# Kernel tuning notes

Hardware: AMD Instinct MI355X
Metric: run time of the kernel (lower is better)

## Reference

```python
import jax, jax.numpy as jnp
import numpy as np
from jax import lax

CHAOS_R = 3.5699456
N_STEPS = 10


def setup_inputs() -> dict:
    key = jax.random.key(0)
    k1, k2, k3 = jax.random.split(key, 3)
    B, T, D = 256, 8192, 5
    x = jax.random.normal(k1, (B, T, D), dtype=jnp.float32)
    temple = jax.random.normal(k2, (4, 5), dtype=jnp.float32)
    breath_vector = jax.random.normal(k3, (5,), dtype=jnp.float32)
    return {"x": x, "temple": temple, "breath_vector": breath_vector}


def reference(x, temple, breath_vector):
    # x: (B, T, D) with D == 5
    B, T, D = x.shape

    # mirror_sequence: chaos logistic map on mean of x[0,0]
    seed = jnp.mod(jnp.mean(x[0, 0]), 1.0)
    chaos = CHAOS_R * seed * (1.0 - seed)
    mirrored = jnp.where(chaos > 0.7, 9.0 - x,
                         jnp.where(chaos > 0.4, jnp.flip(x, axis=1), x))
    mode_code = jnp.where(chaos > 0.7, 0, jnp.where(chaos > 0.4, 1, 2))  # 0=invert,1=retrograde,2=none

    extended_x = jnp.concatenate([x, mirrored], axis=1)  # (B, 2T, D)

    # per-token breath: first T tokens use breath[:4], mirrored half uses breath[1:5]
    breath_main = breath_vector[:4]
    breath_mirror = breath_vector[1:5]
    breath = jnp.concatenate([
        jnp.broadcast_to(breath_main, (T, 4)),
        jnp.broadcast_to(breath_mirror, (T, 4)),
    ], axis=0)  # (2T, 4)

    def step(vec, _):
        # vec: (B, 2T, 5)
        transformed = jnp.einsum('rd,btd->btr', temple, vec)  # (B, 2T, 4)
        resonance = jnp.sum(transformed * breath[None, :, :], axis=-1)  # (B, 2T)
        vec = jnp.roll(vec, shift=1, axis=-1).at[..., 0].set(jnp.mod(resonance, 10.0))
        return vec, resonance

    vec0 = extended_x[..., :5]
    _, history = lax.scan(step, vec0, None, length=N_STEPS)  # (10, B, 2T)

    # torch.std default is unbiased (ddof=1)
    score = 1.0 / (1.0 + jnp.std(history, axis=0, ddof=1))  # (B, 2T)
    gate_weights = score[..., None]  # (B, 2T, 1)
    return gate_weights, extended_x, mode_code
```

## Files before the change

kernel.cpp:

```cpp
#include <hip/hip_runtime.h>

constexpr int B_DIM = 256, T_DIM = 8192;
constexpr long long GATE_N = (long long)B_DIM * 2 * T_DIM;
constexpr long long EXT_N  = GATE_N * 5;

__global__ void temple_setup(const float* __restrict__ x, const float* __restrict__ temple,
                             const float* __restrict__ breath,
                             float* __restrict__ out, double* __restrict__ w) {
    if (threadIdx.x != 0) return;
    double s = 0.0;
    for (int d = 0; d < 5; ++d) s += (double)x[d];
    s = s / 5.0;
    double seed  = s - floor(s);
    double chaos = 3.5699456 * seed * (1.0 - seed);
    int mode = (chaos > 0.7) ? 0 : ((chaos > 0.4) ? 1 : 2);
    for (int d = 0; d < 5; ++d) {
        double a = 0.0, c = 0.0;
        for (int r = 0; r < 4; ++r) {
            double tv = (double)temple[r * 5 + d];
            a += (double)breath[r]     * tv;
            c += (double)breath[r + 1] * tv;
        }
        w[d] = a; w[5 + d] = c;
    }
    w[10] = (double)mode;
    out[GATE_N + EXT_N] = (float)mode;
}

__global__ __launch_bounds__(256) void temple_main(const float* __restrict__ x,
                                                   const double* __restrict__ w,
                                                   float* __restrict__ out) {
    const int k  = threadIdx.x;
    const int b  = blockIdx.x >> 5;
    const int t0 = (blockIdx.x & 31) << 8;
    const int mode = (int)w[10];
    const long long rowBase = (long long)b * (2 * T_DIM);
    float* gate = out;
    float* ext  = out + GATE_N;

    const float4* __restrict__ src4 = (const float4*)(x + ((long long)b * T_DIM + t0) * 5);
    const bool extra = (k < 64);
    float4 c0 = src4[k];
    float4 c1;
    if (extra) c1 = src4[256 + k];

    float4* dmain = (float4*)(ext + (rowBase + t0) * 5);
    dmain[k] = c0;
    if (extra) dmain[256 + k] = c1;
    if (mode == 0) {
        float4* dmir = (float4*)(ext + (rowBase + T_DIM + t0) * 5);
        dmir[k] = make_float4(9.f - c0.x, 9.f - c0.y, 9.f - c0.z, 9.f - c0.w);
        if (extra) dmir[256 + k] = make_float4(9.f - c1.x, 9.f - c1.y, 9.f - c1.z, 9.f - c1.w);
    } else if (mode == 2) {
        float4* dmir = (float4*)(ext + (rowBase + T_DIM + t0) * 5);
        dmir[k] = c0;
        if (extra) dmir[256 + k] = c1;
    }

    const int t = t0 + k;
    const float* __restrict__ xi = x + ((long long)b * T_DIM + t) * 5;
    const float x0 = xi[0], x1 = xi[1], x2 = xi[2], x3 = xi[3], x4 = xi[4];

    if (mode == 1) {
        float* dm = ext + (rowBase + 2 * T_DIM - 1 - t) * 5;
        dm[0] = x0; dm[1] = x1; dm[2] = x2; dm[3] = x3; dm[4] = x4;
    }

    const double wa0 = w[0], wa1 = w[1], wa2 = w[2], wa3 = w[3], wa4 = w[4];
    const double wb0 = w[5], wb1 = w[6], wb2 = w[7], wb3 = w[8], wb4 = w[9];
    double a0 = x0, a1 = x1, a2 = x2, a3 = x3, a4 = x4;
    double b0, b1, b2, b3, b4;
    if (mode == 0) { b0 = 9.0 - a0; b1 = 9.0 - a1; b2 = 9.0 - a2; b3 = 9.0 - a3; b4 = 9.0 - a4; }
    else           { b0 = a0; b1 = a1; b2 = a2; b3 = a3; b4 = a4; }

    float ha[10], hb[10];
#pragma unroll
    for (int s = 0; s < 10; ++s) {
        double ra = a0 * wa0;
        ra = fma(a1, wa1, ra); ra = fma(a2, wa2, ra); ra = fma(a3, wa3, ra); ra = fma(a4, wa4, ra);
        double rb = b0 * wb0;
        rb = fma(b1, wb1, rb); rb = fma(b2, wb2, rb); rb = fma(b3, wb3, rb); rb = fma(b4, wb4, rb);
        ha[s] = (float)ra; hb[s] = (float)rb;
        double qa = floor(ra * 0.1), ma = fma(qa, -10.0, ra);
        ma = (ma < 0.0) ? ma + 10.0 : ma;  ma = (ma >= 10.0) ? ma - 10.0 : ma;
        double qb = floor(rb * 0.1), mb = fma(qb, -10.0, rb);
        mb = (mb < 0.0) ? mb + 10.0 : mb;  mb = (mb >= 10.0) ? mb - 10.0 : mb;
        a4 = a3; a3 = a2; a2 = a1; a1 = a0; a0 = ma;
        b4 = b3; b3 = b2; b2 = b1; b1 = b0; b0 = mb;
    }
    float meanA = 0.f, meanB = 0.f;
#pragma unroll
    for (int s = 0; s < 10; ++s) { meanA += ha[s]; meanB += hb[s]; }
    meanA *= 0.1f; meanB *= 0.1f;
    float ssdA = 0.f, ssdB = 0.f;
#pragma unroll
    for (int s = 0; s < 10; ++s) {
        float da = ha[s] - meanA; ssdA = fmaf(da, da, ssdA);
        float db = hb[s] - meanB; ssdB = fmaf(db, db, ssdB);
    }
    const float gm = 1.0f / (1.0f + sqrtf(ssdA * (1.0f / 9.0f)));
    const float gx = 1.0f / (1.0f + sqrtf(ssdB * (1.0f / 9.0f)));

    gate[rowBase + t] = gm;
    if (mode == 1) gate[rowBase + 2 * T_DIM - 1 - t] = gx;
    else           gate[rowBase + T_DIM + t] = gx;
}

extern "C" void kernel_launch(void* const* d_in, const int* in_sizes, int n_in,
                              void* d_out, int out_size, void* d_ws, size_t ws_size,
                              hipStream_t stream) {
    const float* x      = (const float*)d_in[0];
    const float* temple = (const float*)d_in[1];
    const float* breath = (const float*)d_in[2];
    float* out = (float*)d_out;
    double* w  = (double*)d_ws;

    temple_setup<<<1, 64, 0, stream>>>(x, temple, breath, out, w);
    const int blocks = (B_DIM * T_DIM) / 256;
    temple_main<<<blocks, 256, 0, stream>>>(x, w, out);
}
```

Before: 143.1 us.

## Split copy and gate computation into separate kernels, use one-pass variance

The fused kernel is split in two. One kernel copies the input into the extended output with float4 loads and stores, including a vectorized gather for the retrograde mode. A second kernel computes the gate values. The gate kernel drops the 10-element history arrays and computes variance in one pass from running sum and sum of squares, clamping negatives to zero. This trades an extra launch and a second read of x for simpler kernels with fewer registers, at some risk to numerical accuracy from the one-pass variance formula.

```diff
diff --git a/kernel.cpp b/kernel.cpp
--- a/kernel.cpp
+++ b/kernel.cpp
@@ -27,44 +27,45 @@
     out[GATE_N + EXT_N] = (float)mode;
 }
 
-__global__ __launch_bounds__(256) void temple_main(const float* __restrict__ x,
+__global__ __launch_bounds__(256) void temple_copy(const float* __restrict__ x,
                                                    const double* __restrict__ w,
                                                    float* __restrict__ out) {
-    const int k  = threadIdx.x;
-    const int b  = blockIdx.x >> 5;
-    const int t0 = (blockIdx.x & 31) << 8;
+    const int b = blockIdx.x / 40;
+    const int j = (blockIdx.x - b * 40) * 256 + threadIdx.x;
+    const int mode = (int)w[10];
+
+    const float4 v = ((const float4*)x)[(long long)b * 10240 + j];
+    float4* dst = (float4*)(out + GATE_N) + (long long)b * 20480;
+    dst[j] = v;
+
+    if (mode == 0) {
+        dst[10240 + j] = make_float4(9.f - v.x, 9.f - v.y, 9.f - v.z, 9.f - v.w);
+    } else if (mode == 2) {
+        dst[10240 + j] = v;
+    } else {
+        const float* __restrict__ xr = x + (long long)b * 40960;
+        float vv[4];
+#pragma unroll
+        for (int c = 0; c < 4; ++c) {
+            const int fl = j * 4 + c;
+            const int d  = fl % 5;
+            vv[c] = xr[40955 - fl + 2 * d];
+        }
+        dst[10240 + j] = make_float4(vv[0], vv[1], vv[2], vv[3]);
+    }
+}
+
+__global__ __launch_bounds__(256) void temple_gate(const float* __restrict__ x,
+                                                   const double* __restrict__ w,
+                                                   float* __restrict__ out) {
+    const long long tid = (long long)blockIdx.x * 256 + threadIdx.x;
+    const int b = (int)(tid >> 13);
+    const int t = (int)(tid & (T_DIM - 1));
     const int mode = (int)w[10];
     const long long rowBase = (long long)b * (2 * T_DIM);
-    float* gate = out;
-    float* ext  = out + GATE_N;
 
-    const float4* __restrict__ src4 = (const float4*)(x + ((long long)b * T_DIM + t0) * 5);
-    const bool extra = (k < 64);
-    float4 c0 = src4[k];
-    float4 c1;
-    if (extra) c1 = src4[256 + k];
-
-    float4* dmain = (float4*)(ext + (rowBase + t0) * 5);
-    dmain[k] = c0;
-    if (extra) dmain[256 + k] = c1;
-    if (mode == 0) {
-        float4* dmir = (float4*)(ext + (rowBase + T_DIM + t0) * 5);
-        dmir[k] = make_float4(9.f - c0.x, 9.f - c0.y, 9.f - c0.z, 9.f - c0.w);
-        if (extra) dmir[256 + k] = make_float4(9.f - c1.x, 9.f - c1.y, 9.f - c1.z, 9.f - c1.w);
-    } else if (mode == 2) {
-        float4* dmir = (float4*)(ext + (rowBase + T_DIM + t0) * 5);
-        dmir[k] = c0;
-        if (extra) dmir[256 + k] = c1;
-    }
-
-    const int t = t0 + k;
     const float* __restrict__ xi = x + ((long long)b * T_DIM + t) * 5;
     const float x0 = xi[0], x1 = xi[1], x2 = xi[2], x3 = xi[3], x4 = xi[4];
-
-    if (mode == 1) {
-        float* dm = ext + (rowBase + 2 * T_DIM - 1 - t) * 5;
-        dm[0] = x0; dm[1] = x1; dm[2] = x2; dm[3] = x3; dm[4] = x4;
-    }
 
     const double wa0 = w[0], wa1 = w[1], wa2 = w[2], wa3 = w[3], wa4 = w[4];
     const double wb0 = w[5], wb1 = w[6], wb2 = w[7], wb3 = w[8], wb4 = w[9];
@@ -73,14 +74,16 @@
     if (mode == 0) { b0 = 9.0 - a0; b1 = 9.0 - a1; b2 = 9.0 - a2; b3 = 9.0 - a3; b4 = 9.0 - a4; }
     else           { b0 = a0; b1 = a1; b2 = a2; b3 = a3; b4 = a4; }
 
-    float ha[10], hb[10];
+    float sumA = 0.f, sqA = 0.f, sumB = 0.f, sqB = 0.f;
 #pragma unroll
     for (int s = 0; s < 10; ++s) {
         double ra = a0 * wa0;
         ra = fma(a1, wa1, ra); ra = fma(a2, wa2, ra); ra = fma(a3, wa3, ra); ra = fma(a4, wa4, ra);
         double rb = b0 * wb0;
         rb = fma(b1, wb1, rb); rb = fma(b2, wb2, rb); rb = fma(b3, wb3, rb); rb = fma(b4, wb4, rb);
-        ha[s] = (float)ra; hb[s] = (float)rb;
+        const float fa = (float)ra, fb = (float)rb;
+        sumA += fa; sqA = fmaf(fa, fa, sqA);
+        sumB += fb; sqB = fmaf(fb, fb, sqB);
         double qa = floor(ra * 0.1), ma = fma(qa, -10.0, ra);
         ma = (ma < 0.0) ? ma + 10.0 : ma;  ma = (ma >= 10.0) ? ma - 10.0 : ma;
         double qb = floor(rb * 0.1), mb = fma(qb, -10.0, rb);
@@ -88,22 +91,17 @@
         a4 = a3; a3 = a2; a2 = a1; a1 = a0; a0 = ma;
         b4 = b3; b3 = b2; b2 = b1; b1 = b0; b0 = mb;
     }
-    float meanA = 0.f, meanB = 0.f;
-#pragma unroll
-    for (int s = 0; s < 10; ++s) { meanA += ha[s]; meanB += hb[s]; }
-    meanA *= 0.1f; meanB *= 0.1f;
-    float ssdA = 0.f, ssdB = 0.f;
-#pragma unroll
-    for (int s = 0; s < 10; ++s) {
-        float da = ha[s] - meanA; ssdA = fmaf(da, da, ssdA);
-        float db = hb[s] - meanB; ssdB = fmaf(db, db, ssdB);
-    }
-    const float gm = 1.0f / (1.0f + sqrtf(ssdA * (1.0f / 9.0f)));
-    const float gx = 1.0f / (1.0f + sqrtf(ssdB * (1.0f / 9.0f)));
+    const float meanA = sumA * 0.1f, meanB = sumB * 0.1f;
+    float varA = fmaf(-meanA, sumA, sqA) * (1.0f / 9.0f);
+    float varB = fmaf(-meanB, sumB, sqB) * (1.0f / 9.0f);
+    varA = varA > 0.f ? varA : 0.f;
+    varB = varB > 0.f ? varB : 0.f;
+    const float gm = 1.0f / (1.0f + sqrtf(varA));
+    const float gx = 1.0f / (1.0f + sqrtf(varB));
 
-    gate[rowBase + t] = gm;
-    if (mode == 1) gate[rowBase + 2 * T_DIM - 1 - t] = gx;
-    else           gate[rowBase + T_DIM + t] = gx;
+    out[rowBase + t] = gm;
+    if (mode == 1) out[rowBase + 2 * T_DIM - 1 - t] = gx;
+    else           out[rowBase + T_DIM + t] = gx;
 }
 
 extern "C" void kernel_launch(void* const* d_in, const int* in_sizes, int n_in,
@@ -116,6 +114,6 @@
     double* w  = (double*)d_ws;
 
     temple_setup<<<1, 64, 0, stream>>>(x, temple, breath, out, w);
-    const int blocks = (B_DIM * T_DIM) / 256;
-    temple_main<<<blocks, 256, 0, stream>>>(x, w, out);
+    temple_copy<<<B_DIM * 40, 256, 0, stream>>>(x, w, out);
+    temple_gate<<<(B_DIM * T_DIM) / 256, 256, 0, stream>>>(x, w, out);
 }
```

After: 165.4 us. +15.5%, slower.
